# Kernel optimization log

Measured on AMD Instinct MI355X. Metric: run time of the kernel, lower is better.

Reference implementation:

```python
import jax, jax.numpy as jnp
import numpy as np

N = 20000   # nodes
E = 320000  # edges (avg degree 16)
H = 4       # heads
C = 128     # per-head / output channels (concat=False -> mean over heads)
IN = 2      # init_channels (TSP coords)
NEG_SLOPE = 0.2


def setup_inputs() -> dict:
    key = jax.random.key(0)
    ks = jax.random.split(key, 32)
    s = 0.1
    def W(k, shape):
        return (jax.random.normal(k, shape, jnp.float32) * s)
    inp = {
        "x": jax.random.normal(ks[0], (N, IN), jnp.float32),
        "edge_index": jax.random.randint(ks[1], (2, E), 0, N, jnp.int32),
        "edge_attr": jax.random.uniform(ks[2], (E, 1), jnp.float32),
    }
    i = 3
    for b in range(2):  # two parallel GATBlocks
        inp[f"Wsrc{b}"]  = W(ks[i+0], (IN, H * C))
        inp[f"bsrc{b}"]  = jnp.zeros((H * C,), jnp.float32)
        inp[f"Wdst{b}"]  = W(ks[i+1], (IN, H * C))
        inp[f"bdst{b}"]  = jnp.zeros((H * C,), jnp.float32)
        inp[f"Wedge{b}"] = W(ks[i+2], (1, H * C))
        inp[f"att{b}"]   = W(ks[i+3], (H, C))
        inp[f"bias{b}"]  = jnp.zeros((C,), jnp.float32)
        inp[f"Wres{b}"]  = W(ks[i+4], (IN, C))  # SkipConnection projection (2 -> 128)
        i += 5
    inp["Wfuse"] = W(ks[i], (2 * C, C))
    inp["bfuse"] = jnp.zeros((C,), jnp.float32)
    return inp


def _gat_block(x, src, dst, ea, Wsrc, bsrc, Wdst, bdst, Wedge, att, bias, Wres):
    # GATv2Conv (concat=False) + ReLU + residual projection
    xs = (x @ Wsrc + bsrc).reshape(N, H, C)   # lin_l (source / message)
    xd = (x @ Wdst + bdst).reshape(N, H, C)   # lin_r (target)
    ee = (ea @ Wedge).reshape(-1, H, C)       # lin_edge
    e = jax.nn.leaky_relu(xs[src] + xd[dst] + ee, NEG_SLOPE)  # [Etot,H,C]
    logits = jnp.einsum('ehc,hc->eh', e, att)                 # [Etot,H]
    # segment softmax over incoming edges of each target node
    m = jax.ops.segment_max(logits, dst, num_segments=N)
    m = jnp.where(jnp.isfinite(m), m, 0.0)
    p = jnp.exp(logits - m[dst])
    denom = jax.ops.segment_sum(p, dst, num_segments=N)
    alpha = p / (denom[dst] + 1e-16)                          # [Etot,H]
    agg = jax.ops.segment_sum(xs[src] * alpha[:, :, None], dst, num_segments=N)
    out = agg.mean(axis=1) + bias                             # concat=False: mean heads
    return jax.nn.relu(out) + x @ Wres                        # ReLU then skip add


def reference(x, edge_index, edge_attr,
              Wsrc0, bsrc0, Wdst0, bdst0, Wedge0, att0, bias0, Wres0,
              Wsrc1, bsrc1, Wdst1, bdst1, Wedge1, att1, bias1, Wres1,
              Wfuse, bfuse):
    src, dst = edge_index[0], edge_index[1]
    # PyG default add_self_loops=True, fill_value='mean' for edge_attr
    loop = jnp.arange(N, dtype=src.dtype)
    src_a = jnp.concatenate([src, loop])
    dst_a = jnp.concatenate([dst, loop])
    mean_attr = jnp.mean(edge_attr, axis=0, keepdims=True)
    ea = jnp.concatenate([edge_attr, jnp.broadcast_to(mean_attr, (N, 1))], axis=0)

    h0 = _gat_block(x, src_a, dst_a, ea, Wsrc0, bsrc0, Wdst0, bdst0, Wedge0, att0, bias0, Wres0)
    h1 = _gat_block(x, src_a, dst_a, ea, Wsrc1, bsrc1, Wdst1, bdst1, Wedge1, att1, bias1, Wres1)
    xc = jnp.concatenate([h0, h1], axis=-1)       # [N, 2C]
    return jax.nn.relu(xc @ Wfuse + bfuse)        # [N, C]
```

## Files before the change

kernel.cpp:

```cpp
#include <hip/hip_runtime.h>

#define HH 4
#define CC 128
#define NPB 64

typedef __attribute__((ext_vector_type(8))) short short8v;
typedef __attribute__((ext_vector_type(4))) float f32x4;
typedef _Float16 v2h __attribute__((ext_vector_type(2)));

static inline size_t roundup256(size_t x) { return (x + 255) & ~(size_t)255; }

static __device__ __forceinline__ unsigned short f2bf(float f) {
    unsigned int u = __float_as_uint(f);
    unsigned int r = (u + 0x7FFFu + ((u >> 16) & 1u)) >> 16;
    return (unsigned short)r;
}
static __device__ __forceinline__ v2h bch(unsigned int u) {
    v2h r;
    __builtin_memcpy(&r, &u, 4);
    return r;
}
static __device__ __forceinline__ unsigned int pkh(float a, float b) {
    v2h h = {(_Float16)a, (_Float16)b};
    unsigned int u;
    __builtin_memcpy(&u, &h, 4);
    return u;
}
#if __has_builtin(__builtin_amdgcn_fdot2)
#define FDOT2(a, b, c) __builtin_amdgcn_fdot2((a), (b), (c), false)
#else
#define FDOT2(a, b, c) \
    fmaf((float)(a).x, (float)(b).x, fmaf((float)(a).y, (float)(b).y, (c)))
#endif

__global__ __launch_bounds__(256) void prep_kernel(
    const int* __restrict__ ei, const float* __restrict__ eattr,
    float* __restrict__ meansum, float* __restrict__ Lin, int* __restrict__ cnt,
    const float* __restrict__ Wsrc0, const float* __restrict__ bsrc0,
    const float* __restrict__ Wdst0, const float* __restrict__ bdst0,
    const float* __restrict__ Wedge0, const float* __restrict__ att0,
    const float* __restrict__ Wsrc1, const float* __restrict__ bsrc1,
    const float* __restrict__ Wdst1, const float* __restrict__ bdst1,
    const float* __restrict__ Wedge1, const float* __restrict__ att1,
    const float* __restrict__ Wfuse,
    uint4* __restrict__ pwD, unsigned short* __restrict__ pwB, int E)
{
    int tid = blockIdx.x * 256 + threadIdx.x;
    int lane = threadIdx.x & 63, wid = threadIdx.x >> 6;
    float s = 0.f;
    if (tid < E) {
        atomicAdd(&cnt[ei[E + tid]], 1);
        s = eattr[tid];
    }
    #pragma unroll
    for (int off = 32; off > 0; off >>= 1) s += __shfl_down(s, off, 64);
    __shared__ float wsum[4];
    if (lane == 0) wsum[wid] = s;
    __syncthreads();
    if (threadIdx.x == 0)
        atomicAdd(meansum, wsum[0] + wsum[1] + wsum[2] + wsum[3]);

    if (blockIdx.x < 4) {
        int b = tid >> 9;
        int hc = tid & 511;
        int c = hc & 127;
        int h = hc >> 7;
        int bh = b * 4 + h;
        const float* Ws = b ? Wsrc1 : Wsrc0;
        const float* bs = b ? bsrc1 : bsrc0;
        const float* Wd = b ? Wdst1 : Wdst0;
        const float* bd = b ? bdst1 : bdst0;
        const float* We = b ? Wedge1 : Wedge0;
        const float* at = b ? att1 : att0;
        float A = Ws[hc], B = Ws[512 + hc];
        float C = Wd[hc], D = Wd[512 + hc];
        float Ec = We[hc];
        float F = bs[hc] + bd[hc];
        float a = at[hc];
        pwD[bh * 128 + c] = make_uint4(pkh(A, B), pkh(C, D), pkh(Ec, F),
                                       __float_as_uint(0.4f * a));
        float sa = 0.6f * a;
        float vals[6] = {sa * A, sa * B, sa * C, sa * D, sa * Ec, sa * F};
        #pragma unroll
        for (int k = 0; k < 6; ++k) {
            float v = vals[k];
            #pragma unroll
            for (int off = 32; off > 0; off >>= 1) v += __shfl_down(v, off, 64);
            vals[k] = v;
        }
        __shared__ float Ls[4][6];
        if (lane == 0) {
            #pragma unroll
            for (int k = 0; k < 6; ++k) Ls[wid][k] = vals[k];
        }
        __syncthreads();
        if (threadIdx.x < 12) {
            int w2 = threadIdx.x / 6;
            int k = threadIdx.x % 6;
            int bhg = blockIdx.x * 2 + w2;
            Lin[bhg * 6 + k] = Ls[w2 * 2][k] + Ls[w2 * 2 + 1][k];
        }
    }

    if (blockIdx.x >= 4 && blockIdx.x < 20) {
        int t2 = tid - 1024;
        int ct = t2 >> 9;
        int kc = (t2 >> 6) & 7;
        int l  = t2 & 63;
        int c = ct * 16 + (l & 15);
        int kb = kc * 32 + (l >> 4) * 8;
        unsigned short v[8];
        #pragma unroll
        for (int j = 0; j < 8; ++j)
            v[j] = f2bf(Wfuse[(kb + j) * CC + c]);
        unsigned short* dst = pwB + (size_t)t2 * 8;
        #pragma unroll
        for (int j = 0; j < 8; ++j) dst[j] = v[j];
    }
}

__global__ __launch_bounds__(1024) void scan_kernel(const int* __restrict__ cnt,
                                                    int* __restrict__ rowptr,
                                                    int* __restrict__ cur, int N) {
    const int CH = 32;
    int t = threadIdx.x;
    int base = t * CH;
    int local[CH];
    int s = 0;
    #pragma unroll
    for (int i = 0; i < CH; ++i) {
        int idx = base + i;
        int v = (idx < N) ? cnt[idx] + 1 : 0;
        local[i] = s;
        s += v;
    }
    __shared__ int sums[1024];
    sums[t] = s;
    __syncthreads();
    for (int off = 1; off < 1024; off <<= 1) {
        int v = (t >= off) ? sums[t - off] : 0;
        __syncthreads();
        sums[t] += v;
        __syncthreads();
    }
    int excl = sums[t] - s;
    #pragma unroll
    for (int i = 0; i < CH; ++i) {
        int idx = base + i;
        if (idx < N) {
            int v = excl + local[i];
            rowptr[idx] = v;
            cur[idx] = v;
        }
    }
    if (t == 1023) rowptr[N] = excl + s;
}

__global__ __launch_bounds__(256) void scatter_kernel(
    const int* __restrict__ ei, const float* __restrict__ x,
    const float* __restrict__ eattr, const float* __restrict__ meansum,
    int* __restrict__ cur, float4* __restrict__ ed4, uint4* __restrict__ eh4,
    int N, int E) {
    int e = blockIdx.x * 256 + threadIdx.x;
    int Etot = E + N;
    if (e >= Etot) return;
    int src, dst;
    float ea;
    if (e < E) { src = ei[e]; dst = ei[E + e]; ea = eattr[e]; }
    else       { src = e - E; dst = src; ea = meansum[0] / (float)E; }
    int pos = atomicAdd(&cur[dst], 1);
    const float2* x2 = (const float2*)x;
    float2 xs = x2[src];
    float2 xd = x2[dst];
    ed4[pos] = make_float4(xs.x, xs.y, xd.x, xd.y);
    eh4[pos] = make_uint4(pkh(xs.x, xs.y), pkh(xd.x, xd.y), pkh(ea, 1.f), 0);
}

__global__ __launch_bounds__(256) void logits_kernel(
    const uint4* __restrict__ eh4,
    const float* __restrict__ Lin,
    const uint4* __restrict__ pwD,
    float* __restrict__ p8, int EtotPad, int nchunks)
{
    int blk = blockIdx.x;
    int bh = blk / nchunks;
    int chunk = blk - bh * nchunks;
    int t = threadIdx.x;
    int iA = chunk * 512 + t;
    int iB = iA + 256;
    uint4 eA = eh4[iA], eB = eh4[iB];
    v2h xsA = bch(eA.x), xdA = bch(eA.y), eaA = bch(eA.z);
    v2h xsB = bch(eB.x), xdB = bch(eB.y), eaB = bch(eB.z);

    const uint4* wp = pwD + bh * 128;
    float a0 = 0.f, a1 = 0.f;
    #pragma unroll 8
    for (int c = 0; c < 128; ++c) {
        uint4 w = wp[c];
        v2h AB = bch(w.x), CD = bch(w.y), EF = bch(w.z);
        float G = __uint_as_float(w.w);
        float uA = FDOT2(AB, xsA, FDOT2(CD, xdA, FDOT2(EF, eaA, 0.f)));
        float uB = FDOT2(AB, xsB, FDOT2(CD, xdB, FDOT2(EF, eaB, 0.f)));
        a0 = fmaf(G, __builtin_fabsf(uA), a0);
        a1 = fmaf(G, __builtin_fabsf(uB), a1);
    }

    const float* Lp = Lin + bh * 6;
    float l0 = Lp[0], l1 = Lp[1], l2 = Lp[2], l3 = Lp[3], l4 = Lp[4], l5 = Lp[5];
    float lgA = fmaf(l0, (float)xsA.x, fmaf(l1, (float)xsA.y,
                fmaf(l2, (float)xdA.x, fmaf(l3, (float)xdA.y,
                fmaf(l4, (float)eaA.x, l5))))) + a0;
    float lgB = fmaf(l0, (float)xsB.x, fmaf(l1, (float)xsB.y,
                fmaf(l2, (float)xdB.x, fmaf(l3, (float)xdB.y,
                fmaf(l4, (float)eaB.x, l5))))) + a1;
    float* plane = p8 + (size_t)bh * EtotPad;
    plane[iA] = __expf(lgA);
    plane[iB] = __expf(lgB);
}

__global__ __launch_bounds__(256) void nodeS_kernel(
    const int* __restrict__ rowptr, const float4* __restrict__ ed4,
    const float* __restrict__ p8, float* __restrict__ S, int N, int EtotPad)
{
    int t = threadIdx.x;
    int g = t >> 3, bh = t & 7;
    int n = blockIdx.x * 32 + g;
    if (n >= N) return;
    int beg = rowptr[n], end = rowptr[n + 1];
    const float* plane = p8 + (size_t)bh * EtotPad;
    float s0 = 0.f, s1 = 0.f, sb = 0.f;
    for (int i = beg; i < end; ++i) {
        float4 ed = ed4[i];
        float p = plane[i];
        s0 = fmaf(p, ed.x, s0);
        s1 = fmaf(p, ed.y, s1);
        sb += p;
    }
    float rin = 1.f / (sb + 1e-16f);
    float* Sp = S + (size_t)n * 24 + bh * 3;
    Sp[0] = s0 * rin;
    Sp[1] = s1 * rin;
    Sp[2] = sb * rin;
}

__global__ __launch_bounds__(512) void node_kernel(
    const float* __restrict__ x,
    const float* __restrict__ S,
    const float* __restrict__ Wsrc0, const float* __restrict__ bsrc0,
    const float* __restrict__ bias0, const float* __restrict__ Wres0,
    const float* __restrict__ Wsrc1, const float* __restrict__ bsrc1,
    const float* __restrict__ bias1, const float* __restrict__ Wres1,
    const unsigned short* __restrict__ pwB, const float* __restrict__ bfuse,
    float* __restrict__ out, int N)
{
    __shared__ __align__(16) unsigned short hb[NPB][264];
    int t = threadIdx.x;
    int c = t & (CC - 1);
    int quarter = t >> 7;
    int n0 = blockIdx.x * NPB;

    float w00[HH], w01[HH], wb0[HH], w10[HH], w11[HH], wb1[HH];
    #pragma unroll
    for (int h = 0; h < HH; ++h) {
        w00[h] = Wsrc0[h * CC + c];
        w01[h] = Wsrc0[512 + h * CC + c];
        wb0[h] = bsrc0[h * CC + c];
        w10[h] = Wsrc1[h * CC + c];
        w11[h] = Wsrc1[512 + h * CC + c];
        wb1[h] = bsrc1[h * CC + c];
    }
    float bi0 = bias0[c], bi1 = bias1[c];
    float r00 = Wres0[c], r01 = Wres0[CC + c];
    float r10 = Wres1[c], r11 = Wres1[CC + c];

    for (int ni = quarter; ni < NPB; ni += 4) {
        int n = n0 + ni;
        if (n < N) {
            float x0 = x[2 * n], x1 = x[2 * n + 1];
            const float4* Sp4 = (const float4*)(S + (size_t)n * 24);
            float4 q0 = Sp4[0], q1 = Sp4[1], q2 = Sp4[2];
            float4 q3 = Sp4[3], q4 = Sp4[4], q5 = Sp4[5];
            float h0v, h1v;
            {
                float s0[HH] = {q0.x, q0.w, q1.z, q2.y};
                float s1[HH] = {q0.y, q1.x, q1.w, q2.z};
                float sb[HH] = {q0.z, q1.y, q2.x, q2.w};
                float acc = 0.f;
                #pragma unroll
                for (int h = 0; h < HH; ++h)
                    acc += fmaf(w00[h], s0[h], fmaf(w01[h], s1[h], wb0[h] * sb[h]));
                float o = fmaxf(acc * 0.25f + bi0, 0.f);
                h0v = o + x0 * r00 + x1 * r01;
            }
            {
                float s0[HH] = {q3.x, q3.w, q4.z, q5.y};
                float s1[HH] = {q3.y, q4.x, q4.w, q5.z};
                float sb[HH] = {q3.z, q4.y, q5.x, q5.w};
                float acc = 0.f;
                #pragma unroll
                for (int h = 0; h < HH; ++h)
                    acc += fmaf(w10[h], s0[h], fmaf(w11[h], s1[h], wb1[h] * sb[h]));
                float o = fmaxf(acc * 0.25f + bi1, 0.f);
                h1v = o + x0 * r10 + x1 * r11;
            }
            hb[ni][c] = f2bf(h0v);
            hb[ni][CC + c] = f2bf(h1v);
        }
    }
    __syncthreads();

    int w = t >> 6;
    int l = t & 63;
    int nt = w & 3;
    int cthalf = w >> 2;
    int row = nt * 16 + (l & 15);

    short8v a[8];
    #pragma unroll
    for (int kc = 0; kc < 8; ++kc)
        a[kc] = *reinterpret_cast<const short8v*>(&hb[row][kc * 32 + (l >> 4) * 8]);

    const short8v* pB = reinterpret_cast<const short8v*>(pwB);
    #pragma unroll
    for (int ci = 0; ci < 4; ++ci) {
        int ct = cthalf * 4 + ci;
        f32x4 acc = {0.f, 0.f, 0.f, 0.f};
        #pragma unroll
        for (int kc = 0; kc < 8; ++kc) {
            short8v b = pB[(ct * 8 + kc) * 64 + l];
            acc = __builtin_amdgcn_mfma_f32_16x16x32_bf16(a[kc], b, acc, 0, 0, 0);
        }
        int ch = ct * 16 + (l & 15);
        float bi = bfuse[ch];
        #pragma unroll
        for (int j = 0; j < 4; ++j) {
            int n = n0 + nt * 16 + (l >> 4) * 4 + j;
            if (n < N) out[(size_t)n * CC + ch] = fmaxf(acc[j] + bi, 0.f);
        }
    }
}

extern "C" void kernel_launch(void* const* d_in, const int* in_sizes, int n_in,
                              void* d_out, int out_size, void* d_ws, size_t ws_size,
                              hipStream_t stream) {
    const float* x      = (const float*)d_in[0];
    const int*   ei     = (const int*)d_in[1];
    const float* eattr  = (const float*)d_in[2];
    const float* Wsrc0  = (const float*)d_in[3];
    const float* bsrc0  = (const float*)d_in[4];
    const float* Wdst0  = (const float*)d_in[5];
    const float* bdst0  = (const float*)d_in[6];
    const float* Wedge0 = (const float*)d_in[7];
    const float* att0   = (const float*)d_in[8];
    const float* bias0  = (const float*)d_in[9];
    const float* Wres0  = (const float*)d_in[10];
    const float* Wsrc1  = (const float*)d_in[11];
    const float* bsrc1  = (const float*)d_in[12];
    const float* Wdst1  = (const float*)d_in[13];
    const float* bdst1  = (const float*)d_in[14];
    const float* Wedge1 = (const float*)d_in[15];
    const float* att1   = (const float*)d_in[16];
    const float* bias1  = (const float*)d_in[17];
    const float* Wres1  = (const float*)d_in[18];
    const float* Wfuse  = (const float*)d_in[19];
    const float* bfuse  = (const float*)d_in[20];
    float* out = (float*)d_out;

    int N = in_sizes[0] / 2;
    int E = in_sizes[1] / 2;
    int Etot = E + N;
    int EtotPad = (Etot + 511) & ~511;

    size_t off = 0;
    float* meansum = (float*)((char*)d_ws + off);  off += 256;
    int*   cnt     = (int*)((char*)d_ws + off);    off += roundup256((size_t)N * sizeof(int));
    size_t zero_bytes = off;
    float* Lin     = (float*)((char*)d_ws + off);  off += 256;
    int*   cur     = (int*)((char*)d_ws + off);    off += roundup256((size_t)N * sizeof(int));
    int*   rowptr  = (int*)((char*)d_ws + off);    off += roundup256((size_t)(N + 1) * sizeof(int));
    uint4* pwD     = (uint4*)((char*)d_ws + off);  off += roundup256(1024 * sizeof(uint4));
    unsigned short* pwB = (unsigned short*)((char*)d_ws + off);
                                                   off += roundup256(4096 * 8 * sizeof(unsigned short));
    float4* ed4    = (float4*)((char*)d_ws + off); off += roundup256((size_t)EtotPad * sizeof(float4));
    uint4* eh4     = (uint4*)((char*)d_ws + off);  off += roundup256((size_t)EtotPad * sizeof(uint4));
    float* p8      = (float*)((char*)d_ws + off);  off += roundup256((size_t)EtotPad * 8 * sizeof(float));
    float* S       = (float*)((char*)d_ws + off);  off += roundup256((size_t)24 * N * sizeof(float));

    hipMemsetAsync(d_ws, 0, zero_bytes, stream);

    prep_kernel<<<(E + 255) / 256, 256, 0, stream>>>(
        ei, eattr, meansum, Lin, cnt,
        Wsrc0, bsrc0, Wdst0, bdst0, Wedge0, att0,
        Wsrc1, bsrc1, Wdst1, bdst1, Wedge1, att1,
        Wfuse, pwD, pwB, E);

    scan_kernel<<<1, 1024, 0, stream>>>(cnt, rowptr, cur, N);

    scatter_kernel<<<(Etot + 255) / 256, 256, 0, stream>>>(
        ei, x, eattr, meansum, cur, ed4, eh4, N, E);

    int nchunks = EtotPad / 512;
    logits_kernel<<<8 * nchunks, 256, 0, stream>>>(
        eh4, Lin, pwD, p8, EtotPad, nchunks);

    nodeS_kernel<<<(N + 31) / 32, 256, 0, stream>>>(rowptr, ed4, p8, S, N, EtotPad);

    node_kernel<<<(N + NPB - 1) / NPB, 512, 0, stream>>>(
        x, S,
        Wsrc0, bsrc0, bias0, Wres0,
        Wsrc1, bsrc1, bias1, Wres1,
        pwB, bfuse, out, N);
}
```

Baseline: 182.6 us.

## Fuse per-node softmax reduction into node kernel and drop ed4 buffer

Removes the separate nodeS kernel and the S intermediate by computing per-node normalized sums inside node_kernel into shared memory. Source index is packed into eh4's spare word so source coords are gathered from x instead of a stored ed4 array, removing one edge-sized write. The logits kernel now handles two block-heads per block and writes p8 interleaved edge-major so the node reduction reads contiguous 8-float groups. The trade-off is scattered gathers of x in node_kernel, a second half-wave of 8-lane strided p8 writes in logits, and a serial reduction stage before the node compute.

```diff
diff --git a/kernel.cpp b/kernel.cpp
--- a/kernel.cpp
+++ b/kernel.cpp
@@ -159,8 +159,7 @@
 __global__ __launch_bounds__(256) void scatter_kernel(
     const int* __restrict__ ei, const float* __restrict__ x,
     const float* __restrict__ eattr, const float* __restrict__ meansum,
-    int* __restrict__ cur, float4* __restrict__ ed4, uint4* __restrict__ eh4,
-    int N, int E) {
+    int* __restrict__ cur, uint4* __restrict__ eh4, int N, int E) {
     int e = blockIdx.x * 256 + threadIdx.x;
     int Etot = E + N;
     if (e >= Etot) return;
@@ -172,19 +171,19 @@
     const float2* x2 = (const float2*)x;
     float2 xs = x2[src];
     float2 xd = x2[dst];
-    ed4[pos] = make_float4(xs.x, xs.y, xd.x, xd.y);
-    eh4[pos] = make_uint4(pkh(xs.x, xs.y), pkh(xd.x, xd.y), pkh(ea, 1.f), 0);
+    eh4[pos] = make_uint4(pkh(xs.x, xs.y), pkh(xd.x, xd.y), pkh(ea, 1.f),
+                          (unsigned)src);
 }
 
 __global__ __launch_bounds__(256) void logits_kernel(
     const uint4* __restrict__ eh4,
     const float* __restrict__ Lin,
     const uint4* __restrict__ pwD,
-    float* __restrict__ p8, int EtotPad, int nchunks)
+    float* __restrict__ p8, int nchunks)
 {
     int blk = blockIdx.x;
-    int bh = blk / nchunks;
-    int chunk = blk - bh * nchunks;
+    int bhp = blk / nchunks;
+    int chunk = blk - bhp * nchunks;
     int t = threadIdx.x;
     int iA = chunk * 512 + t;
     int iB = iA + 256;
@@ -192,60 +191,39 @@
     v2h xsA = bch(eA.x), xdA = bch(eA.y), eaA = bch(eA.z);
     v2h xsB = bch(eB.x), xdB = bch(eB.y), eaB = bch(eB.z);
 
-    const uint4* wp = pwD + bh * 128;
-    float a0 = 0.f, a1 = 0.f;
-    #pragma unroll 8
-    for (int c = 0; c < 128; ++c) {
-        uint4 w = wp[c];
-        v2h AB = bch(w.x), CD = bch(w.y), EF = bch(w.z);
-        float G = __uint_as_float(w.w);
-        float uA = FDOT2(AB, xsA, FDOT2(CD, xdA, FDOT2(EF, eaA, 0.f)));
-        float uB = FDOT2(AB, xsB, FDOT2(CD, xdB, FDOT2(EF, eaB, 0.f)));
-        a0 = fmaf(G, __builtin_fabsf(uA), a0);
-        a1 = fmaf(G, __builtin_fabsf(uB), a1);
-    }
-
-    const float* Lp = Lin + bh * 6;
-    float l0 = Lp[0], l1 = Lp[1], l2 = Lp[2], l3 = Lp[3], l4 = Lp[4], l5 = Lp[5];
-    float lgA = fmaf(l0, (float)xsA.x, fmaf(l1, (float)xsA.y,
-                fmaf(l2, (float)xdA.x, fmaf(l3, (float)xdA.y,
-                fmaf(l4, (float)eaA.x, l5))))) + a0;
-    float lgB = fmaf(l0, (float)xsB.x, fmaf(l1, (float)xsB.y,
-                fmaf(l2, (float)xdB.x, fmaf(l3, (float)xdB.y,
-                fmaf(l4, (float)eaB.x, l5))))) + a1;
-    float* plane = p8 + (size_t)bh * EtotPad;
-    plane[iA] = __expf(lgA);
-    plane[iB] = __expf(lgB);
-}
-
-__global__ __launch_bounds__(256) void nodeS_kernel(
-    const int* __restrict__ rowptr, const float4* __restrict__ ed4,
-    const float* __restrict__ p8, float* __restrict__ S, int N, int EtotPad)
-{
-    int t = threadIdx.x;
-    int g = t >> 3, bh = t & 7;
-    int n = blockIdx.x * 32 + g;
-    if (n >= N) return;
-    int beg = rowptr[n], end = rowptr[n + 1];
-    const float* plane = p8 + (size_t)bh * EtotPad;
-    float s0 = 0.f, s1 = 0.f, sb = 0.f;
-    for (int i = beg; i < end; ++i) {
-        float4 ed = ed4[i];
-        float p = plane[i];
-        s0 = fmaf(p, ed.x, s0);
-        s1 = fmaf(p, ed.y, s1);
-        sb += p;
-    }
-    float rin = 1.f / (sb + 1e-16f);
-    float* Sp = S + (size_t)n * 24 + bh * 3;
-    Sp[0] = s0 * rin;
-    Sp[1] = s1 * rin;
-    Sp[2] = sb * rin;
+    #pragma unroll
+    for (int bi = 0; bi < 2; ++bi) {
+        int bh = bhp * 2 + bi;
+        const uint4* wp = pwD + bh * 128;
+        float a0 = 0.f, a1 = 0.f;
+        #pragma unroll 8
+        for (int c = 0; c < 128; ++c) {
+            uint4 w = wp[c];
+            v2h AB = bch(w.x), CD = bch(w.y), EF = bch(w.z);
+            float G = __uint_as_float(w.w);
+            float uA = FDOT2(AB, xsA, FDOT2(CD, xdA, FDOT2(EF, eaA, 0.f)));
+            float uB = FDOT2(AB, xsB, FDOT2(CD, xdB, FDOT2(EF, eaB, 0.f)));
+            a0 = fmaf(G, __builtin_fabsf(uA), a0);
+            a1 = fmaf(G, __builtin_fabsf(uB), a1);
+        }
+        const float* Lp = Lin + bh * 6;
+        float l0 = Lp[0], l1 = Lp[1], l2 = Lp[2], l3 = Lp[3], l4 = Lp[4], l5 = Lp[5];
+        float lgA = fmaf(l0, (float)xsA.x, fmaf(l1, (float)xsA.y,
+                    fmaf(l2, (float)xdA.x, fmaf(l3, (float)xdA.y,
+                    fmaf(l4, (float)eaA.x, l5))))) + a0;
+        float lgB = fmaf(l0, (float)xsB.x, fmaf(l1, (float)xsB.y,
+                    fmaf(l2, (float)xdB.x, fmaf(l3, (float)xdB.y,
+                    fmaf(l4, (float)eaB.x, l5))))) + a1;
+        p8[(size_t)iA * 8 + bh] = __expf(lgA);
+        p8[(size_t)iB * 8 + bh] = __expf(lgB);
+    }
 }
 
 __global__ __launch_bounds__(512) void node_kernel(
     const float* __restrict__ x,
-    const float* __restrict__ S,
+    const int* __restrict__ rowptr,
+    const uint4* __restrict__ eh4,
+    const float* __restrict__ p8,
     const float* __restrict__ Wsrc0, const float* __restrict__ bsrc0,
     const float* __restrict__ bias0, const float* __restrict__ Wres0,
     const float* __restrict__ Wsrc1, const float* __restrict__ bsrc1,
@@ -254,10 +232,35 @@
     float* __restrict__ out, int N)
 {
     __shared__ __align__(16) unsigned short hb[NPB][264];
+    __shared__ __align__(16) float Sl[NPB][24];
     int t = threadIdx.x;
+    int n0 = blockIdx.x * NPB;
+    const float2* x2 = (const float2*)x;
+
+    {
+        int g = t >> 3, bh = t & 7;
+        int n = n0 + g;
+        if (n < N) {
+            int beg = rowptr[n], end = rowptr[n + 1];
+            float s0 = 0.f, s1 = 0.f, sb = 0.f;
+            for (int i = beg; i < end; ++i) {
+                float p = p8[(size_t)i * 8 + bh];
+                unsigned srcu = eh4[i].w;
+                float2 xs = x2[srcu];
+                s0 = fmaf(p, xs.x, s0);
+                s1 = fmaf(p, xs.y, s1);
+                sb += p;
+            }
+            float rin = 1.f / (sb + 1e-16f);
+            Sl[g][bh * 3 + 0] = s0 * rin;
+            Sl[g][bh * 3 + 1] = s1 * rin;
+            Sl[g][bh * 3 + 2] = sb * rin;
+        }
+    }
+    __syncthreads();
+
     int c = t & (CC - 1);
     int quarter = t >> 7;
-    int n0 = blockIdx.x * NPB;
 
     float w00[HH], w01[HH], wb0[HH], w10[HH], w11[HH], wb1[HH];
     #pragma unroll
@@ -277,7 +280,7 @@
         int n = n0 + ni;
         if (n < N) {
             float x0 = x[2 * n], x1 = x[2 * n + 1];
-            const float4* Sp4 = (const float4*)(S + (size_t)n * 24);
+            const float4* Sp4 = (const float4*)&Sl[ni][0];
             float4 q0 = Sp4[0], q1 = Sp4[1], q2 = Sp4[2];
             float4 q3 = Sp4[3], q4 = Sp4[4], q5 = Sp4[5];
             float h0v, h1v;
@@ -381,10 +384,8 @@
     uint4* pwD     = (uint4*)((char*)d_ws + off);  off += roundup256(1024 * sizeof(uint4));
     unsigned short* pwB = (unsigned short*)((char*)d_ws + off);
                                                    off += roundup256(4096 * 8 * sizeof(unsigned short));
-    float4* ed4    = (float4*)((char*)d_ws + off); off += roundup256((size_t)EtotPad * sizeof(float4));
     uint4* eh4     = (uint4*)((char*)d_ws + off);  off += roundup256((size_t)EtotPad * sizeof(uint4));
     float* p8      = (float*)((char*)d_ws + off);  off += roundup256((size_t)EtotPad * 8 * sizeof(float));
-    float* S       = (float*)((char*)d_ws + off);  off += roundup256((size_t)24 * N * sizeof(float));
 
     hipMemsetAsync(d_ws, 0, zero_bytes, stream);
 
@@ -397,16 +398,14 @@
     scan_kernel<<<1, 1024, 0, stream>>>(cnt, rowptr, cur, N);
 
     scatter_kernel<<<(Etot + 255) / 256, 256, 0, stream>>>(
-        ei, x, eattr, meansum, cur, ed4, eh4, N, E);
+        ei, x, eattr, meansum, cur, eh4, N, E);
 
     int nchunks = EtotPad / 512;
-    logits_kernel<<<8 * nchunks, 256, 0, stream>>>(
-        eh4, Lin, pwD, p8, EtotPad, nchunks);
-
-    nodeS_kernel<<<(N + 31) / 32, 256, 0, stream>>>(rowptr, ed4, p8, S, N, EtotPad);
+    logits_kernel<<<4 * nchunks, 256, 0, stream>>>(
+        eh4, Lin, pwD, p8, nchunks);
 
     node_kernel<<<(N + NPB - 1) / NPB, 512, 0, stream>>>(
-        x, S,
+        x, rowptr, eh4, p8,
         Wsrc0, bsrc0, bias0, Wres0,
         Wsrc1, bsrc1, bias1, Wres1,
         pwB, bfuse, out, N);
```

Result: faster. 175.0 us (-4.1%).
